# Optimization experiments

Hardware: AMD Instinct MI355X
Metric: run time of the kernel (lower is better)

## Reference

```python
import jax, jax.numpy as jnp
import numpy as np

DT = 1.0
SPIKE_THRESHOLD = 30.0


def setup_inputs() -> dict:
    key = jax.random.key(0)
    kx, = jax.random.split(key, 1)
    x = jax.random.normal(kx, (16, 64, 1024, 32), dtype=jnp.float32)
    # scalar learnable parameters (Izhikevich model constants)
    a = jnp.float32(0.02)
    b = jnp.float32(0.2)
    c = jnp.float32(-65.0)
    d = jnp.float32(8.0)
    return {"x": x, "a": a, "b": b, "c": c, "d": d}


def reference(x, a, b, c, d):
    # x: [B, C, N, T]. Initial membrane potential v and recovery u are zeros.
    B, C, N, T = x.shape
    v0 = jnp.zeros((B, C, N), dtype=x.dtype)
    u0 = jnp.zeros((B, C, N), dtype=x.dtype)
    xs = jnp.moveaxis(x, -1, 0)  # [T, B, C, N] time-major for scan

    def step(carry, x_t):
        v, u = carry
        dv = 0.04 * v * v + 5.0 * v + 140.0 - u + x_t
        v = v + DT * dv
        du = a * (b * v - u)
        u = u + DT * du
        spike = (v >= SPIKE_THRESHOLD).astype(x_t.dtype)
        v = v * (1.0 - spike) + c * spike
        u = u + d * spike
        return (v, u), spike

    (_, _), spikes = jax.lax.scan(step, (v0, u0), xs)
    return jnp.moveaxis(spikes, 0, -1)  # [B, C, N, T]
```

## Files before the change

### kernel.cpp

```cpp
#include <hip/hip_runtime.h>


#define T_STEPS 32
#define TPB 64
#define ROW 36
#define NT 4

#define LGKM_ONLY 0xC07F

typedef float vf4 __attribute__((ext_vector_type(4)));

__global__ __launch_bounds__(TPB) void izhikevich_kernel(
    const float* __restrict__ x,
    const float* __restrict__ pa,
    const float* __restrict__ pb,
    const float* __restrict__ pc,
    const float* __restrict__ pd,
    float* __restrict__ out)
{
#pragma clang fp contract(off)
    __shared__ float lds[TPB * ROW];

    const int t = threadIdx.x;
    const size_t tile_elems = (size_t)TPB * T_STEPS;
    const size_t base0 = (size_t)blockIdx.x * (NT * tile_elems);

    const float a = pa[0];
    const float b = pb[0];
    const float c = pc[0];
    const float d = pd[0];

    vf4 ch[8];
    {
        const vf4* __restrict__ xin = reinterpret_cast<const vf4*>(x + base0);
#pragma unroll
        for (int k = 0; k < 8; ++k) ch[k] = xin[k * TPB + t];
    }

#pragma unroll
    for (int it = 0; it < NT; ++it) {
        vf4 chn[8];
        if (it + 1 < NT) {
            const vf4* __restrict__ xin = reinterpret_cast<const vf4*>(
                x + base0 + (size_t)(it + 1) * tile_elems);
#pragma unroll
            for (int k = 0; k < 8; ++k) chn[k] = xin[k * TPB + t];
        }
        __builtin_amdgcn_sched_barrier(0);

#pragma unroll
        for (int k = 0; k < 8; ++k) {
            const int ng = k * 8 + (t >> 3);
            const int tg = (t & 7) * 4;
            *reinterpret_cast<vf4*>(&lds[ng * ROW + tg]) = ch[k];
        }
        __builtin_amdgcn_s_waitcnt(LGKM_ONLY);
        __builtin_amdgcn_sched_barrier(0);

        float v = 0.0f;
        float u = 0.0f;
#pragma unroll
        for (int j = 0; j < 8; ++j) {
            const vf4 xv = *reinterpret_cast<const vf4*>(&lds[t * ROW + j * 4]);
            vf4 sp;
#pragma unroll
            for (int i = 0; i < 4; ++i) {
                const float xt = xv[i];
                const float t1 = (0.04f * v) * v;
                const float t2 = 5.0f * v;
                const float dv = (((t1 + t2) + 140.0f) - u) + xt;
                v = v + dv;
                const float du = a * ((b * v) - u);
                u = u + du;
                const float spike = (v >= 30.0f) ? 1.0f : 0.0f;
                const float oms = 1.0f - spike;
                v = (v * oms) + (c * spike);
                u = u + (d * spike);
                sp[i] = spike;
            }
            *reinterpret_cast<vf4*>(&lds[t * ROW + j * 4]) = sp;
        }
        __builtin_amdgcn_s_waitcnt(LGKM_ONLY);
        __builtin_amdgcn_sched_barrier(0);

        {
            vf4* __restrict__ op =
                reinterpret_cast<vf4*>(out + base0 + (size_t)it * tile_elems);
#pragma unroll
            for (int k = 0; k < 8; ++k) {
                const int ng = k * 8 + (t >> 3);
                const int tg = (t & 7) * 4;
                const vf4 o = *reinterpret_cast<const vf4*>(&lds[ng * ROW + tg]);
                __builtin_nontemporal_store(o, op + k * TPB + t);
            }
        }
        __builtin_amdgcn_sched_barrier(0);

        if (it + 1 < NT) {
#pragma unroll
            for (int k = 0; k < 8; ++k) ch[k] = chn[k];
        }
    }
}

extern "C" void kernel_launch(void* const* d_in, const int* in_sizes, int n_in,
                              void* d_out, int out_size, void* d_ws, size_t ws_size,
                              hipStream_t stream) {
    const float* x  = (const float*)d_in[0];
    const float* pa = (const float*)d_in[1];
    const float* pb = (const float*)d_in[2];
    const float* pc = (const float*)d_in[3];
    const float* pd = (const float*)d_in[4];
    float* out = (float*)d_out;

    const int n_neurons = in_sizes[0] / T_STEPS;
    const int grid = n_neurons / (TPB * NT);

    izhikevich_kernel<<<grid, TPB, 0, stream>>>(x, pa, pb, pc, pd, out);
}
```

Measured before the change: 241.2 us.

## Pack spikes into bitmasks, transpose via bpermute, use 4-wave blocks

Spike outputs are now packed into a 32-bit mask per neuron and redistributed across lanes with ds_bpermute instead of being written back to LDS and re-read for the transpose. Each output store is delayed into the next iteration so it overlaps with the following tile's load. Blocks now hold four independent waves, each with its own LDS slice, which cuts the block count and changes occupancy. The bit-unpack adds a few ALU ops per store in exchange for fewer LDS round trips.

After: 248.9 us. +3.2%, slower.

```diff
diff --git a/kernel.cpp b/kernel.cpp
--- a/kernel.cpp
+++ b/kernel.cpp
@@ -1,16 +1,20 @@
 #include <hip/hip_runtime.h>
+#include <stdint.h>
 
 
 #define T_STEPS 32
-#define TPB 64
+#define WV 64
+#define WAVES 4
+#define TPB (WV * WAVES)
+#define NT 4
 #define ROW 36
-#define NT 4
-
-#define LGKM_ONLY 0xC07F
+#define TILE_F 2048
 
 typedef float vf4 __attribute__((ext_vector_type(4)));
 
-__global__ __launch_bounds__(TPB) void izhikevich_kernel(
+#define WLGKM0 0xC07F
+
+__global__ __launch_bounds__(TPB, 4) void izhikevich_kernel(
     const float* __restrict__ x,
     const float* __restrict__ pa,
     const float* __restrict__ pb,
@@ -19,32 +23,63 @@
     float* __restrict__ out)
 {
 #pragma clang fp contract(off)
-    __shared__ float lds[TPB * ROW];
+    __shared__ float lds[WAVES * WV * ROW];
 
-    const int t = threadIdx.x;
-    const size_t tile_elems = (size_t)TPB * T_STEPS;
-    const size_t base0 = (size_t)blockIdx.x * (NT * tile_elems);
+    const int tid = threadIdx.x;
+    const int t = tid & 63;
+    const int w = tid >> 6;
+    float* __restrict__ wlds = &lds[w * WV * ROW];
+
+    const size_t wave_base = (size_t)blockIdx.x * (WAVES * NT * (size_t)TILE_F)
+                           + (size_t)w * (NT * (size_t)TILE_F);
+    const float* __restrict__ xw = x + wave_base;
+    float* __restrict__ ow = out + wave_base;
 
     const float a = pa[0];
     const float b = pb[0];
     const float c = pc[0];
     const float d = pd[0];
 
+    const int sh = (t & 7) << 2;
+    const int bpaddr = ((t >> 3) << 2);
+
     vf4 ch[8];
     {
-        const vf4* __restrict__ xin = reinterpret_cast<const vf4*>(x + base0);
+        const vf4* __restrict__ xin = reinterpret_cast<const vf4*>(xw);
 #pragma unroll
-        for (int k = 0; k < 8; ++k) ch[k] = xin[k * TPB + t];
+        for (int k = 0; k < 8; ++k) ch[k] = xin[k * WV + t];
+#pragma unroll
+        for (int k = 0; k < 8; ++k) asm volatile("" : "+v"(ch[k]));
     }
 
+    unsigned nw[8];
+
 #pragma unroll
-    for (int it = 0; it < NT; ++it) {
+    for (int i = 0; i < NT; ++i) {
+        if (i > 0) {
+            vf4* __restrict__ op =
+                reinterpret_cast<vf4*>(ow + (size_t)(i - 1) * TILE_F);
+#pragma unroll
+            for (int kk = 0; kk < 8; ++kk) {
+                const unsigned nib = (nw[kk] >> sh) & 0xFu;
+                vf4 o;
+                o.x = (nib & 1u) ? 1.0f : 0.0f;
+                o.y = (nib & 2u) ? 1.0f : 0.0f;
+                o.z = (nib & 4u) ? 1.0f : 0.0f;
+                o.w = (nib & 8u) ? 1.0f : 0.0f;
+                __builtin_nontemporal_store(o, op + kk * WV + t);
+            }
+        }
+        __builtin_amdgcn_sched_barrier(0);
+
         vf4 chn[8];
-        if (it + 1 < NT) {
-            const vf4* __restrict__ xin = reinterpret_cast<const vf4*>(
-                x + base0 + (size_t)(it + 1) * tile_elems);
+        if (i + 1 < NT) {
+            const vf4* __restrict__ xin =
+                reinterpret_cast<const vf4*>(xw + (size_t)(i + 1) * TILE_F);
 #pragma unroll
-            for (int k = 0; k < 8; ++k) chn[k] = xin[k * TPB + t];
+            for (int k = 0; k < 8; ++k) chn[k] = xin[k * WV + t];
+#pragma unroll
+            for (int k = 0; k < 8; ++k) asm volatile("" : "+v"(chn[k]));
         }
         __builtin_amdgcn_sched_barrier(0);
 
@@ -52,53 +87,58 @@
         for (int k = 0; k < 8; ++k) {
             const int ng = k * 8 + (t >> 3);
             const int tg = (t & 7) * 4;
-            *reinterpret_cast<vf4*>(&lds[ng * ROW + tg]) = ch[k];
+            *reinterpret_cast<vf4*>(&wlds[ng * ROW + tg]) = ch[k];
         }
-        __builtin_amdgcn_s_waitcnt(LGKM_ONLY);
+        __builtin_amdgcn_s_waitcnt(WLGKM0);
         __builtin_amdgcn_sched_barrier(0);
 
-        float v = 0.0f;
-        float u = 0.0f;
+        float v = 0.0f, u = 0.0f;
+        unsigned pk = 0u;
 #pragma unroll
-        for (int j = 0; j < 8; ++j) {
-            const vf4 xv = *reinterpret_cast<const vf4*>(&lds[t * ROW + j * 4]);
-            vf4 sp;
+        for (int g = 0; g < 8; ++g) {
+            const vf4 xg = *reinterpret_cast<const vf4*>(&wlds[t * ROW + g * 4]);
 #pragma unroll
-            for (int i = 0; i < 4; ++i) {
-                const float xt = xv[i];
+            for (int ii = 0; ii < 4; ++ii) {
+                const float xt = xg[ii];
                 const float t1 = (0.04f * v) * v;
                 const float t2 = 5.0f * v;
                 const float dv = (((t1 + t2) + 140.0f) - u) + xt;
                 v = v + dv;
                 const float du = a * ((b * v) - u);
                 u = u + du;
-                const float spike = (v >= 30.0f) ? 1.0f : 0.0f;
+                const bool sb = (v >= 30.0f);
+                const float spike = sb ? 1.0f : 0.0f;
+                pk |= sb ? (1u << (4 * g + ii)) : 0u;
                 const float oms = 1.0f - spike;
                 v = (v * oms) + (c * spike);
                 u = u + (d * spike);
-                sp[i] = spike;
             }
-            *reinterpret_cast<vf4*>(&lds[t * ROW + j * 4]) = sp;
         }
-        __builtin_amdgcn_s_waitcnt(LGKM_ONLY);
+
+#pragma unroll
+        for (int kk = 0; kk < 8; ++kk)
+            nw[kk] = (unsigned)__builtin_amdgcn_ds_bpermute(
+                (kk << 5) + bpaddr, (int)pk);
         __builtin_amdgcn_sched_barrier(0);
 
-        {
-            vf4* __restrict__ op =
-                reinterpret_cast<vf4*>(out + base0 + (size_t)it * tile_elems);
-#pragma unroll
-            for (int k = 0; k < 8; ++k) {
-                const int ng = k * 8 + (t >> 3);
-                const int tg = (t & 7) * 4;
-                const vf4 o = *reinterpret_cast<const vf4*>(&lds[ng * ROW + tg]);
-                __builtin_nontemporal_store(o, op + k * TPB + t);
-            }
-        }
-        __builtin_amdgcn_sched_barrier(0);
-
-        if (it + 1 < NT) {
+        if (i + 1 < NT) {
 #pragma unroll
             for (int k = 0; k < 8; ++k) ch[k] = chn[k];
+        }
+    }
+
+    {
+        vf4* __restrict__ op =
+            reinterpret_cast<vf4*>(ow + (size_t)(NT - 1) * TILE_F);
+#pragma unroll
+        for (int kk = 0; kk < 8; ++kk) {
+            const unsigned nib = (nw[kk] >> sh) & 0xFu;
+            vf4 o;
+            o.x = (nib & 1u) ? 1.0f : 0.0f;
+            o.y = (nib & 2u) ? 1.0f : 0.0f;
+            o.z = (nib & 4u) ? 1.0f : 0.0f;
+            o.w = (nib & 8u) ? 1.0f : 0.0f;
+            __builtin_nontemporal_store(o, op + kk * WV + t);
         }
     }
 }
@@ -114,7 +154,7 @@
     float* out = (float*)d_out;
 
     const int n_neurons = in_sizes[0] / T_STEPS;
-    const int grid = n_neurons / (TPB * NT);
+    const int grid = n_neurons / (WAVES * NT * WV);
 
     izhikevich_kernel<<<grid, TPB, 0, stream>>>(x, pa, pb, pc, pd, out);
 }
```
